# Optimization experiments

Measured on AMD Instinct MI355X. Metric: run time of the kernel, lower is better.

Reference implementation:

```python
import jax, jax.numpy as jnp
import numpy as np
from jax import lax

BETA = 0.5        # Sinkhron beta
N_ITER = 20       # got_iteration
THRESH = 0.1      # P > 0.1 threshold
NL_I = 5          # apply_non_linearity(..., 'elu', i=5)
EPS = 1e-9


def setup_inputs() -> dict:
    key = jax.random.key(0)
    k1, k2 = jax.random.split(key)
    B, N, D = 128, 512, 128
    h = jax.random.normal(k1, (B, N, D), dtype=jnp.float32)
    W0 = jnp.ones((D,), dtype=jnp.float32)
    W1 = jnp.ones((D,), dtype=jnp.float32)
    lengths = jax.random.randint(k2, (B,), 0, N, dtype=jnp.int32)
    return {"h": h, "W0": W0, "W1": W1, "lengths": lengths}


def _forward(h, W0, W1, lengths):
    B, N, D = h.shape
    lengths = jnp.maximum(lengths, 1)
    mask = (jnp.arange(N)[None, :] < lengths[:, None])          # [B, N] bool
    mf = mask.astype(h.dtype)
    mask2 = mf[:, :, None] * mf[:, None, :]                      # [B, N, N]

    # internal_forward: Diag layers with relu between (mlp_act='relu')
    h = h * W0
    h = jax.nn.relu(h)
    h = h * W1

    # cost_matrix_batch_torch: cosine similarity, add identity diag, mask
    hn = h / (jnp.linalg.norm(h, axis=-1, keepdims=True) + 1e-12)
    sim = jnp.einsum('bnd,bmd->bnm', hn, hn)                     # [B, N, N]
    sim = sim + jnp.eye(N, dtype=h.dtype)                        # add_eye_diag
    sim = sim * mask2
    cost = (1.0 - sim) * mask2

    # Sinkhorn with uniform marginals on valid nodes, fixed iterations
    n = lengths.astype(h.dtype)
    mu = mf / n[:, None]                                         # [B, N]
    K = jnp.exp(-cost / BETA) * mask2                            # [B, N, N]

    def body(carry, _):
        u, v = carry
        u = mu / (jnp.einsum('bnm,bm->bn', K, v) + EPS) * mf
        v = mu / (jnp.einsum('bnm,bn->bm', K, u) + EPS) * mf
        return (u, v), None

    (u, v), _ = lax.scan(body, (mf, mf), None, length=N_ITER)
    P = u[:, :, None] * K * v[:, None, :]                        # transport plan

    # P.detach(); scale by number of nodes per graph; threshold
    P = lax.stop_gradient(P)
    P = n[:, None, None] * P
    A = (P > THRESH).astype(h.dtype)
    similarity = A * sim
    # apply_non_linearity 'elu': elu(x*i - i) + 1
    out = jax.nn.elu(similarity * NL_I - NL_I) + 1.0
    return out


def reference(h, W0, W1, lengths):
    return _forward(h, W0, W1, lengths)
```

## Files before the change

### kernel.cpp

```cpp
#include <hip/hip_runtime.h>

#define BB 128
#define NN 512
#define DD 128

__global__ __launch_bounds__(256) void hn_kernel(const float* __restrict__ h,
                                                 const float* __restrict__ W0,
                                                 const float* __restrict__ W1,
                                                 float* __restrict__ hn) {
    int wave = (int)((blockIdx.x * blockDim.x + threadIdx.x) >> 6);
    int lane = threadIdx.x & 63;
    const float2* h2 = (const float2*)(h + (size_t)wave * DD);
    float2 w0 = ((const float2*)W0)[lane];
    float2 w1 = ((const float2*)W1)[lane];
    float2 x = h2[lane];
    float p0 = fmaxf(x.x * w0.x, 0.0f) * w1.x;
    float p1 = fmaxf(x.y * w0.y, 0.0f) * w1.y;
    float ss = p0 * p0 + p1 * p1;
#pragma unroll
    for (int m = 32; m; m >>= 1) ss += __shfl_xor(ss, m);
    float inv = 1.0f / (sqrtf(ss) + 1e-12f);
    float2 o;
    o.x = p0 * inv;
    o.y = p1 * inv;
    ((float2*)(hn + (size_t)wave * DD))[lane] = o;
}

#define KC 32
__global__ __launch_bounds__(256) void sim_kernel(const float* __restrict__ hn,
                                                  const int* __restrict__ lengths,
                                                  float* __restrict__ K) {
    __shared__ float As[KC][132];
    __shared__ float Bs[KC][132];
    __shared__ int pre[BB + 1];
    int tid = threadIdx.x;
    if (tid == 0) {
        int acc = 0;
        for (int b = 0; b < BB; b++) {
            pre[b] = acc;
            int len = max(lengths[b], 1);
            int nt = (len + 127) >> 7;
            acc += nt * (nt + 1) / 2;
        }
        pre[BB] = acc;
    }
    __syncthreads();
    int total = pre[BB];

    int lr = tid >> 3;
    int lk = (tid & 7) << 2;
    int tx = tid & 15, ty = tid >> 4;

    for (int t = blockIdx.x; t < total; t += gridDim.x) {
        int lo = 0, hi = BB;
        while (lo + 1 < hi) {
            int mid = (lo + hi) >> 1;
            if (pre[mid] <= t) lo = mid; else hi = mid;
        }
        int b = lo;
        int local = t - pre[b];
        int len = max(lengths[b], 1);
        int nt = (len + 127) >> 7;
        int ti = 0, rem = local;
        while (rem >= nt - ti) { rem -= nt - ti; ti++; }
        int tj = ti + rem;
        int r0 = ti << 7, c0 = tj << 7;
        const float* base = hn + (size_t)b * NN * DD;
        float acc[8][8] = {};

        for (int kc = 0; kc < DD; kc += KC) {
#pragma unroll
            for (int rr = 0; rr < 128; rr += 32) {
                float4 a = *(const float4*)(base + (size_t)(r0 + lr + rr) * DD + kc + lk);
                As[lk + 0][lr + rr] = a.x; As[lk + 1][lr + rr] = a.y;
                As[lk + 2][lr + rr] = a.z; As[lk + 3][lr + rr] = a.w;
                float4 bb = *(const float4*)(base + (size_t)(c0 + lr + rr) * DD + kc + lk);
                Bs[lk + 0][lr + rr] = bb.x; Bs[lk + 1][lr + rr] = bb.y;
                Bs[lk + 2][lr + rr] = bb.z; Bs[lk + 3][lr + rr] = bb.w;
            }
            __syncthreads();
#pragma unroll
            for (int kk = 0; kk < KC; kk++) {
                float4 a0 = *(const float4*)&As[kk][ty * 8];
                float4 a1 = *(const float4*)&As[kk][ty * 8 + 4];
                float4 b0 = *(const float4*)&Bs[kk][tx * 4];
                float4 b1 = *(const float4*)&Bs[kk][64 + tx * 4];
                float ar[8] = {a0.x, a0.y, a0.z, a0.w, a1.x, a1.y, a1.z, a1.w};
                float bc[8] = {b0.x, b0.y, b0.z, b0.w, b1.x, b1.y, b1.z, b1.w};
#pragma unroll
                for (int r = 0; r < 8; r++)
#pragma unroll
                    for (int c = 0; c < 8; c++)
                        acc[r][c] = fmaf(ar[r], bc[c], acc[r][c]);
            }
            __syncthreads();
        }
        float* out = K + (size_t)b * NN * NN;
#pragma unroll
        for (int r = 0; r < 8; r++) {
            int i = r0 + ty * 8 + r;
            if (i >= len) continue;
#pragma unroll
            for (int cg = 0; cg < 2; cg++) {
                int j0 = c0 + cg * 64 + tx * 4;
                if (j0 >= len) continue;
                float vv[4];
#pragma unroll
                for (int c = 0; c < 4; c++) {
                    float s = acc[r][cg * 4 + c] + ((i == j0 + c) ? 1.0f : 0.0f);
                    vv[c] = expf(2.0f * s - 2.0f);
                }
                float4 o;
                o.x = vv[0]; o.y = vv[1]; o.z = vv[2]; o.w = vv[3];
                *(float4*)(out + (size_t)i * NN + j0) = o;
            }
        }
        if (ti != tj) {
#pragma unroll
            for (int cg = 0; cg < 2; cg++) {
                for (int half = 0; half < 2; half++) {
                    __syncthreads();
                    if ((tx >> 3) == half) {
                        int jl = (tx & 7) * 4;
#pragma unroll
                        for (int r = 0; r < 8; r++)
#pragma unroll
                            for (int c = 0; c < 4; c++)
                                As[jl + c][ty * 8 + r] = acc[r][cg * 4 + c];
                    }
                    __syncthreads();
                    int jrow = tid >> 3;
                    int j = c0 + cg * 64 + half * 32 + jrow;
                    if (j < len) {
                        int ib = (tid & 7) * 16;
#pragma unroll
                        for (int s4 = 0; s4 < 4; s4++) {
                            int il = ib + s4 * 4;
                            int i0 = r0 + il;
                            if (i0 >= len) continue;
                            float4 sraw = *(const float4*)&As[jrow][il];
                            float4 o;
                            o.x = expf(2.0f * sraw.x - 2.0f);
                            o.y = expf(2.0f * sraw.y - 2.0f);
                            o.z = expf(2.0f * sraw.z - 2.0f);
                            o.w = expf(2.0f * sraw.w - 2.0f);
                            *(float4*)(out + (size_t)j * NN + i0) = o;
                        }
                    }
                }
            }
            __syncthreads();
        }
    }
}

__device__ __forceinline__ float dot8(float4 A, float4 B, float4 x0, float4 x1) {
    float d = fmaf(A.x, x0.x, fmaf(A.y, x0.y, fmaf(A.z, x0.z, A.w * x0.w)));
    return fmaf(B.x, x1.x, fmaf(B.y, x1.y, fmaf(B.z, x1.z, fmaf(B.w, x1.w, d))));
}

#define ROWS22(X) X(0) X(1) X(2) X(3) X(4) X(5) X(6) X(7) X(8) X(9) X(10) \
    X(11) X(12) X(13) X(14) X(15) X(16) X(17) X(18) X(19) X(20) X(21)

__global__ __launch_bounds__(512, 2) void coop_sink(const float* __restrict__ K,
                                                    float* __restrict__ u_buf,
                                                    float* __restrict__ v_buf,
                                                    const int* __restrict__ lengths,
                                                    unsigned long long* __restrict__ slots64) {
    __shared__ float xb[NN];
    __shared__ float pv[8 * NN];
    __shared__ int Sh[BB], Pre[BB];

    int g = blockIdx.x;
    int tid = threadIdx.x;

    if (tid == 0) {
        int need[BB]; int ssum = 0;
        for (int m = 0; m < BB; m++) {
            int L = max(lengths[m], 1);
            need[m] = (L + 175) / 176;
            ssum += need[m];
        }
        while (ssum > 256) {
            int best = 0, bv = need[0];
            for (int m = 1; m < BB; m++)
                if (need[m] > bv) { bv = need[m]; best = m; }
            need[best]--; ssum--;
        }
        int acc = 0;
        for (int m = 0; m < BB; m++) { Pre[m] = acc; Sh[m] = need[m]; acc += need[m]; }
    }
    __syncthreads();

    int m = -1;
    for (int mm = 0; mm < BB; mm++)
        if (g >= Pre[mm] && g < Pre[mm] + Sh[mm]) { m = mm; break; }
    if (m < 0) return;
    int b = m;
    int jbase = Pre[m];
    int q = g - jbase;
    int S = Sh[m];

    int len = max(lengths[b], 1);
    int len4 = (len + 3) & ~3;
    int rpq = (len + S - 1) / S;
    int r_lo = q * rpq;
    int nrows = min(len - r_lo, rpq);
    if (nrows < 0) nrows = 0;
    float inv_n = 1.0f / (float)len;

    int w = tid >> 6, l = tid & 63;
    int c0 = 4 * l, c1 = 256 + 4 * l;
    bool a0 = c0 < len4, a1 = c1 < len4;
    const float* Kb = K + (size_t)b * NN * NN;

    xb[tid] = (tid < len) ? 1.0f : 0.0f;

#define DECL(o) float4 kA##o = {0,0,0,0}, kB##o = {0,0,0,0};
    ROWS22(DECL)
#undef DECL
#define FILL_ROW(o)                                                          \
    {                                                                        \
        int i_ = w + 8 * (o);                                                \
        if (i_ < nrows) {                                                    \
            const float* g0_ = Kb + (size_t)(r_lo + i_) * NN;                \
            if (a0) kA##o = *(const float4*)(g0_ + c0);                      \
            if (a1) kB##o = *(const float4*)(g0_ + c1);                      \
        }                                                                    \
    }
    ROWS22(FILL_ROW)
#undef FILL_ROW

    __syncthreads();

    for (int t = 0; t < 20; t++) {
        float4 xv0 = *(const float4*)(xb + c0);
        float4 xv1 = *(const float4*)(xb + c1);
        float4 pa = {0, 0, 0, 0}, pb = {0, 0, 0, 0};

#define DOT(o) float d##o = dot8(kA##o, kB##o, xv0, xv1);
        ROWS22(DOT)
#undef DOT
#pragma unroll
        for (int mm2 = 32; mm2; mm2 >>= 1) {
#define BF(o) d##o += __shfl_xor(d##o, mm2);
            ROWS22(BF)
#undef BF
        }
#define RC(o) float uu##o = inv_n / (d##o + 1e-9f);
        ROWS22(RC)
#undef RC
#define ACC_ROW(o)                                                           \
    pa.x = fmaf(kA##o.x, uu##o, pa.x); pa.y = fmaf(kA##o.y, uu##o, pa.y);    \
    pa.z = fmaf(kA##o.z, uu##o, pa.z); pa.w = fmaf(kA##o.w, uu##o, pa.w);    \
    pb.x = fmaf(kB##o.x, uu##o, pb.x); pb.y = fmaf(kB##o.y, uu##o, pb.y);    \
    pb.z = fmaf(kB##o.z, uu##o, pb.z); pb.w = fmaf(kB##o.w, uu##o, pb.w);
        ROWS22(ACC_ROW)
#undef ACC_ROW
        if (t == 19 && l == 0) {
            float* ub = u_buf + (size_t)b * NN + r_lo + w;
#define ST(o) if (w + 8 * (o) < nrows) ub[8 * (o)] = uu##o;
            ROWS22(ST)
#undef ST
        }

        for (int i = 176 + w; i < nrows; i += 8) {
            const float* g0 = Kb + (size_t)(r_lo + i) * NN;
            float4 A = {0, 0, 0, 0}, B = {0, 0, 0, 0};
            if (a0) A = *(const float4*)(g0 + c0);
            if (a1) B = *(const float4*)(g0 + c1);
            float d = dot8(A, B, xv0, xv1);
#pragma unroll
            for (int mm2 = 32; mm2; mm2 >>= 1) d += __shfl_xor(d, mm2);
            float uu = inv_n / (d + 1e-9f);
            pa.x = fmaf(A.x, uu, pa.x); pa.y = fmaf(A.y, uu, pa.y);
            pa.z = fmaf(A.z, uu, pa.z); pa.w = fmaf(A.w, uu, pa.w);
            pb.x = fmaf(B.x, uu, pb.x); pb.y = fmaf(B.y, uu, pb.y);
            pb.z = fmaf(B.z, uu, pb.z); pb.w = fmaf(B.w, uu, pb.w);
            if (t == 19 && l == 0) u_buf[(size_t)b * NN + r_lo + i] = uu;
        }

        *(float4*)(pv + w * NN + c0) = pa;
        *(float4*)(pv + w * NN + c1) = pb;
        __syncthreads();
        int c = tid;
        float s0 = pv[c] + pv[NN + c] + pv[2 * NN + c] + pv[3 * NN + c] +
                   pv[4 * NN + c] + pv[5 * NN + c] + pv[6 * NN + c] + pv[7 * NN + c];
        unsigned long long* pbase =
            slots64 + ((size_t)(t & 1) * 512) * 512;
        if (S > 1) {
            unsigned long long pk =
                ((unsigned long long)(unsigned)(t + 1) << 32) | __float_as_uint(s0);
            __hip_atomic_store(pbase + (size_t)g * 512 + c, pk,
                               __ATOMIC_RELAXED, __HIP_MEMORY_SCOPE_AGENT);
        }

        float t0 = s0;
        for (int s = 1; s < S; s++) {
            int k = q + s; if (k >= S) k -= S;
            const unsigned long long* p64 = pbase + (size_t)(jbase + k) * 512 + c;
            unsigned long long vpk =
                __hip_atomic_load(p64, __ATOMIC_RELAXED, __HIP_MEMORY_SCOPE_AGENT);
            while ((unsigned)(vpk >> 32) != (unsigned)(t + 1)) {
                __builtin_amdgcn_s_sleep(1);
                vpk = __hip_atomic_load(p64, __ATOMIC_RELAXED, __HIP_MEMORY_SCOPE_AGENT);
            }
            t0 += __uint_as_float((unsigned)vpk);
        }
        float v0 = (c < len) ? (inv_n / (t0 + 1e-9f)) : 0.0f;
        if (t < 19) {
            xb[c] = v0;
        } else if (c >= r_lo && c < r_lo + nrows) {
            v_buf[(size_t)b * NN + c] = v0;
        }
        __syncthreads();
    }
}

__global__ __launch_bounds__(256) void epi_kernel(float* __restrict__ io,
                                                  const float* __restrict__ u,
                                                  const float* __restrict__ v,
                                                  const int* __restrict__ lengths) {
    const float E5 = 0.006737946999085467f;
    size_t idx = (size_t)blockIdx.x * 256 + threadIdx.x;
    int b = (int)(idx >> 16);
    int r = (int)(idx >> 7) & (NN - 1);
    int c4 = ((int)idx & 127) << 2;
    int len = max(lengths[b], 1);
    float4 o;
    if (r >= len || c4 >= len) {
        o.x = E5; o.y = E5; o.z = E5; o.w = E5;
        ((float4*)io)[idx] = o;
        return;
    }
    float4 k = ((float4*)io)[idx];
    float ui = u[(size_t)b * NN + r];
    float4 vv = *(const float4*)(v + (size_t)b * NN + c4);
    float t = (float)len * ui;
    float kv[4] = {k.x, k.y, k.z, k.w};
    float vj[4] = {vv.x, vv.y, vv.z, vv.w};
    float ov[4];
#pragma unroll
    for (int c = 0; c < 4; c++) {
        float Kc = kv[c];
        float P = t * Kc * vj[c];
        bool valid = (c4 + c) < len;
        if (valid && P > 0.1f) {
            float x = 2.5f * logf(Kc);
            ov[c] = (x > 0.0f) ? (x + 1.0f) : expf(x);
        } else {
            ov[c] = E5;
        }
    }
    o.x = ov[0]; o.y = ov[1]; o.z = ov[2]; o.w = ov[3];
    ((float4*)io)[idx] = o;
}

extern "C" void kernel_launch(void* const* d_in, const int* in_sizes, int n_in,
                              void* d_out, int out_size, void* d_ws, size_t ws_size,
                              hipStream_t stream) {
    const float* h = (const float*)d_in[0];
    const float* W0 = (const float*)d_in[1];
    const float* W1 = (const float*)d_in[2];
    const int* lengths = (const int*)d_in[3];
    float* K = (float*)d_out;

    char* ws = (char*)d_ws;
    float* hn = (float*)ws;
    size_t off = (size_t)BB * NN * DD * 4;
    float* u = (float*)(ws + off); off += (size_t)BB * NN * 4;
    float* v = (float*)(ws + off); off += (size_t)BB * NN * 4;
    unsigned long long* slots64 = (unsigned long long*)(ws + off);
    off += (size_t)2 * 512 * 512 * 8;

    hn_kernel<<<BB * NN / 4, 256, 0, stream>>>(h, W0, W1, hn);
    sim_kernel<<<1024, 256, 0, stream>>>(hn, lengths, K);

    coop_sink<<<256, 512, 0, stream>>>(K, u, v, lengths, slots64);

    epi_kernel<<<(unsigned)((size_t)BB * NN * NN / 4 / 256), 256, 0, stream>>>(K, u, v, lengths);
}
```

Baseline: 358.5 us.

## Hold up to 256 rows in registers and split each batch across at most two blocks

Each wave now keeps 32 rows of K in registers instead of 22, so one block can hold 256 rows. The global-memory loop for rows past that limit is removed. The load-balancing scheduler is replaced by a fixed rule: a batch uses two blocks if its length is over 256, otherwise one. This cuts cross-block synchronisation to a single partner and avoids reloading K every iteration. The cost is much higher register pressure, since about 256 VGPRs go to K alone, which risks spills. The hint for two blocks per CU is also dropped, and long batches get less parallelism.

```diff
diff --git a/kernel.cpp b/kernel.cpp
--- a/kernel.cpp
+++ b/kernel.cpp
@@ -159,14 +159,15 @@
     return fmaf(B.x, x1.x, fmaf(B.y, x1.y, fmaf(B.z, x1.z, fmaf(B.w, x1.w, d))));
 }
 
-#define ROWS22(X) X(0) X(1) X(2) X(3) X(4) X(5) X(6) X(7) X(8) X(9) X(10) \
-    X(11) X(12) X(13) X(14) X(15) X(16) X(17) X(18) X(19) X(20) X(21)
-
-__global__ __launch_bounds__(512, 2) void coop_sink(const float* __restrict__ K,
-                                                    float* __restrict__ u_buf,
-                                                    float* __restrict__ v_buf,
-                                                    const int* __restrict__ lengths,
-                                                    unsigned long long* __restrict__ slots64) {
+#define ROWS32(X) X(0) X(1) X(2) X(3) X(4) X(5) X(6) X(7) X(8) X(9) X(10) \
+    X(11) X(12) X(13) X(14) X(15) X(16) X(17) X(18) X(19) X(20) X(21) X(22) \
+    X(23) X(24) X(25) X(26) X(27) X(28) X(29) X(30) X(31)
+
+__global__ __launch_bounds__(512) void coop_sink(const float* __restrict__ K,
+                                                 float* __restrict__ u_buf,
+                                                 float* __restrict__ v_buf,
+                                                 const int* __restrict__ lengths,
+                                                 unsigned long long* __restrict__ slots64) {
     __shared__ float xb[NN];
     __shared__ float pv[8 * NN];
     __shared__ int Sh[BB], Pre[BB];
@@ -175,20 +176,12 @@
     int tid = threadIdx.x;
 
     if (tid == 0) {
-        int need[BB]; int ssum = 0;
+        int acc = 0;
         for (int m = 0; m < BB; m++) {
             int L = max(lengths[m], 1);
-            need[m] = (L + 175) / 176;
-            ssum += need[m];
-        }
-        while (ssum > 256) {
-            int best = 0, bv = need[0];
-            for (int m = 1; m < BB; m++)
-                if (need[m] > bv) { bv = need[m]; best = m; }
-            need[best]--; ssum--;
-        }
-        int acc = 0;
-        for (int m = 0; m < BB; m++) { Pre[m] = acc; Sh[m] = need[m]; acc += need[m]; }
+            int S = (L > 256) ? 2 : 1;
+            Pre[m] = acc; Sh[m] = S; acc += S;
+        }
     }
     __syncthreads();
 
@@ -217,18 +210,18 @@
     xb[tid] = (tid < len) ? 1.0f : 0.0f;
 
 #define DECL(o) float4 kA##o = {0,0,0,0}, kB##o = {0,0,0,0};
-    ROWS22(DECL)
+    ROWS32(DECL)
 #undef DECL
-#define FILL_ROW(o)                                                          \
-    {                                                                        \
-        int i_ = w + 8 * (o);                                                \
-        if (i_ < nrows) {                                                    \
-            const float* g0_ = Kb + (size_t)(r_lo + i_) * NN;                \
-            if (a0) kA##o = *(const float4*)(g0_ + c0);                      \
-            if (a1) kB##o = *(const float4*)(g0_ + c1);                      \
-        }                                                                    \
-    }
-    ROWS22(FILL_ROW)
+#define FILL_ROW(o)                                                         \
+    {                                                                       \
+        int i_ = w + 8 * (o);                                               \
+        if (i_ < nrows) {                                                   \
+            const float* g0_ = Kb + (size_t)(r_lo + i_) * NN;               \
+            if (a0) kA##o = *(const float4*)(g0_ + c0);                     \
+            if (a1) kB##o = *(const float4*)(g0_ + c1);                     \
+        }                                                                   \
+    }
+    ROWS32(FILL_ROW)
 #undef FILL_ROW
 
     __syncthreads();
@@ -239,45 +232,29 @@
         float4 pa = {0, 0, 0, 0}, pb = {0, 0, 0, 0};
 
 #define DOT(o) float d##o = dot8(kA##o, kB##o, xv0, xv1);
-        ROWS22(DOT)
+        ROWS32(DOT)
 #undef DOT
 #pragma unroll
         for (int mm2 = 32; mm2; mm2 >>= 1) {
 #define BF(o) d##o += __shfl_xor(d##o, mm2);
-            ROWS22(BF)
+            ROWS32(BF)
 #undef BF
         }
 #define RC(o) float uu##o = inv_n / (d##o + 1e-9f);
-        ROWS22(RC)
+        ROWS32(RC)
 #undef RC
-#define ACC_ROW(o)                                                           \
-    pa.x = fmaf(kA##o.x, uu##o, pa.x); pa.y = fmaf(kA##o.y, uu##o, pa.y);    \
-    pa.z = fmaf(kA##o.z, uu##o, pa.z); pa.w = fmaf(kA##o.w, uu##o, pa.w);    \
-    pb.x = fmaf(kB##o.x, uu##o, pb.x); pb.y = fmaf(kB##o.y, uu##o, pb.y);    \
+#define ACC_ROW(o)                                                          \
+    pa.x = fmaf(kA##o.x, uu##o, pa.x); pa.y = fmaf(kA##o.y, uu##o, pa.y);   \
+    pa.z = fmaf(kA##o.z, uu##o, pa.z); pa.w = fmaf(kA##o.w, uu##o, pa.w);   \
+    pb.x = fmaf(kB##o.x, uu##o, pb.x); pb.y = fmaf(kB##o.y, uu##o, pb.y);   \
     pb.z = fmaf(kB##o.z, uu##o, pb.z); pb.w = fmaf(kB##o.w, uu##o, pb.w);
-        ROWS22(ACC_ROW)
+        ROWS32(ACC_ROW)
 #undef ACC_ROW
         if (t == 19 && l == 0) {
             float* ub = u_buf + (size_t)b * NN + r_lo + w;
 #define ST(o) if (w + 8 * (o) < nrows) ub[8 * (o)] = uu##o;
-            ROWS22(ST)
+            ROWS32(ST)
 #undef ST
-        }
-
-        for (int i = 176 + w; i < nrows; i += 8) {
-            const float* g0 = Kb + (size_t)(r_lo + i) * NN;
-            float4 A = {0, 0, 0, 0}, B = {0, 0, 0, 0};
-            if (a0) A = *(const float4*)(g0 + c0);
-            if (a1) B = *(const float4*)(g0 + c1);
-            float d = dot8(A, B, xv0, xv1);
-#pragma unroll
-            for (int mm2 = 32; mm2; mm2 >>= 1) d += __shfl_xor(d, mm2);
-            float uu = inv_n / (d + 1e-9f);
-            pa.x = fmaf(A.x, uu, pa.x); pa.y = fmaf(A.y, uu, pa.y);
-            pa.z = fmaf(A.z, uu, pa.z); pa.w = fmaf(A.w, uu, pa.w);
-            pb.x = fmaf(B.x, uu, pb.x); pb.y = fmaf(B.y, uu, pb.y);
-            pb.z = fmaf(B.z, uu, pb.z); pb.w = fmaf(B.w, uu, pb.w);
-            if (t == 19 && l == 0) u_buf[(size_t)b * NN + r_lo + i] = uu;
         }
 
         *(float4*)(pv + w * NN + c0) = pa;
@@ -296,9 +273,9 @@
         }
 
         float t0 = s0;
-        for (int s = 1; s < S; s++) {
-            int k = q + s; if (k >= S) k -= S;
-            const unsigned long long* p64 = pbase + (size_t)(jbase + k) * 512 + c;
+        if (S > 1) {
+            const unsigned long long* p64 =
+                pbase + (size_t)(jbase + (1 - q)) * 512 + c;
             unsigned long long vpk =
                 __hip_atomic_load(p64, __ATOMIC_RELAXED, __HIP_MEMORY_SCOPE_AGENT);
             while ((unsigned)(vpk >> 32) != (unsigned)(t + 1)) {
```

Result: slower. 626.6 us (+74.8%).
